# Kernel optimization log

Measured on AMD Instinct MI355X. Metric: run time of the kernel, lower is better.

Reference implementation:

```python
import jax, jax.numpy as jnp
import numpy as np

B, T, NF, T2V, GH, NH, GRUH = 128, 256, 17, 16, 32, 4, 128


def _t2v(t, w0, b0, W, Bp):
    # t: [...] -> [..., T2V] = [linear term, sin periodic terms]
    lin = t[..., None] * w0 + b0
    per = jnp.sin(t[..., None] * W + Bp)
    return jnp.concatenate([lin, per], axis=-1)


def _gat(h, adj, W, a_src, a_dst, residual):
    # h: [N, F, Din], W: [Din, H, O], a_*: [H, O]; batched multi-head GAT over N graphs
    p = jnp.einsum('nfd,dho->nfho', h, W)
    es = jnp.einsum('nfho,ho->nhf', p, a_src)
    ed = jnp.einsum('nfho,ho->nhf', p, a_dst)
    e = jax.nn.leaky_relu(es[:, :, :, None] + ed[:, :, None, :], 0.2)  # [N,H,F,F]
    e = jnp.where(adj[None, None] > 0, e, jnp.float32(-1e9))
    a = jax.nn.softmax(e, axis=-1)
    out = jnp.einsum('nhij,njho->niho', a, p).reshape(h.shape[0], h.shape[1], -1)
    if residual:
        out = out + h
    return jax.nn.elu(out)


def _gru_dir(x, wih, whh, bih, bhh, reverse):
    # PyTorch GRU gate order [r, z, n]; x: [B,T,D] -> (outputs [B,T,H], h_final [B,H])
    gx = jnp.einsum('btd,gd->btg', x, wih) + bih
    if reverse:
        gx = gx[:, ::-1]
    H = whh.shape[1]

    def step(h, gxt):
        gh = h @ whh.T + bhh
        r = jax.nn.sigmoid(gxt[:, :H] + gh[:, :H])
        z = jax.nn.sigmoid(gxt[:, H:2 * H] + gh[:, H:2 * H])
        n = jnp.tanh(gxt[:, 2 * H:] + r * gh[:, 2 * H:])
        h2 = (1.0 - z) * n + z * h
        return h2, h2

    h0 = jnp.zeros((x.shape[0], H), x.dtype)
    hT, ys = jax.lax.scan(step, h0, jnp.swapaxes(gx, 0, 1))
    ys = jnp.swapaxes(ys, 0, 1)
    if reverse:
        ys = ys[:, ::-1]
    return ys, hT


def setup_inputs() -> dict:
    key = jax.random.key(0)
    ks = iter(jax.random.split(key, 64))

    def nrm(shape, fan):
        return jax.random.normal(next(ks), shape, jnp.float32) / np.float32(np.sqrt(fan))

    X = jax.random.normal(next(ks), (B, T, NF), jnp.float32)
    mask = (jax.random.uniform(next(ks), (B, T, NF)) > 0.3).astype(jnp.float32)
    delta = jax.random.uniform(next(ks), (B, T, NF), jnp.float32) * 10.0
    times = jnp.broadcast_to(jnp.arange(T, dtype=jnp.float32)[None], (B, T)) + jax.random.uniform(next(ks), (B, T), jnp.float32)
    adj = jnp.ones((NF, NF), jnp.float32) - jnp.eye(NF, dtype=jnp.float32)

    D0 = 2 + 2 * T2V  # node_in_dim = 34
    GO = GH * NH      # gat_out_dim = 128
    inp = dict(X=X, mask=mask, delta=delta, times=times, adj=adj,
               aw0=nrm((1,), 1), ab0=nrm((1,), 1), aW=nrm((T2V - 1,), 1), aB=nrm((T2V - 1,), 1),
               dw0=nrm((1,), 1), db0=nrm((1,), 1), dW=nrm((T2V - 1,), 1), dB=nrm((T2V - 1,), 1),
               gW0=nrm((D0, NH, GH), D0), gas0=nrm((NH, GH), GH), gad0=nrm((NH, GH), GH),
               gW1=nrm((GO, NH, GH), GO), gas1=nrm((NH, GH), GH), gad1=nrm((NH, GH), GH))
    for name, ind in [('g0f', GO), ('g0b', GO), ('g1f', 2 * GRUH), ('g1b', 2 * GRUH)]:
        inp[name + '_wih'] = nrm((3 * GRUH, ind), ind)
        inp[name + '_whh'] = nrm((3 * GRUH, GRUH), GRUH)
        inp[name + '_bih'] = jnp.zeros((3 * GRUH,), jnp.float32)
        inp[name + '_bhh'] = jnp.zeros((3 * GRUH,), jnp.float32)
    pd = 2 * GRUH
    inp.update(mh_w1=nrm((64, pd), pd), mh_b1=jnp.zeros((64,), jnp.float32),
               mh_w2=nrm((1, 64), 64), mh_b2=jnp.zeros((1,), jnp.float32),
               ch_w1=nrm((64, pd), pd), ch_b1=jnp.zeros((64,), jnp.float32),
               ch_w2=nrm((1, 64), 64), ch_b2=jnp.zeros((1,), jnp.float32))
    return inp


def reference(X, mask, delta, times, adj, aw0, ab0, aW, aB, dw0, db0, dW, dB,
              gW0, gas0, gad0, gW1, gas1, gad1,
              g0f_wih, g0f_whh, g0f_bih, g0f_bhh, g0b_wih, g0b_whh, g0b_bih, g0b_bhh,
              g1f_wih, g1f_whh, g1f_bih, g1f_bhh, g1b_wih, g1b_whh, g1b_bih, g1b_bhh,
              mh_w1, mh_b1, mh_w2, mh_b2, ch_w1, ch_b1, ch_w2, ch_b2):
    Bx, Tx, F = X.shape
    # node features: [x, mask, time2vec(t), time2vec(delta)] -> [B,T,F,34]
    t_emb = _t2v(times, aw0, ab0, aW, aB)
    t_emb = jnp.broadcast_to(t_emb[:, :, None, :], (Bx, Tx, F, T2V))
    d_emb = _t2v(delta, dw0, db0, dW, dB)
    nf = jnp.concatenate([X[..., None], mask[..., None], t_emb, d_emb], axis=-1)
    # batched GAT over all B*T graphs at once (replaces the Python bt-loop)
    h = nf.reshape(Bx * Tx, F, nf.shape[-1])
    h = _gat(h, adj, gW0, gas0, gad0, False)
    h = _gat(h, adj, gW1, gas1, gad1, True)
    z = h.mean(axis=1).reshape(Bx, Tx, NH * GH)
    # bidirectional 2-layer GRU
    yf, _ = _gru_dir(z, g0f_wih, g0f_whh, g0f_bih, g0f_bhh, False)
    yb, _ = _gru_dir(z, g0b_wih, g0b_whh, g0b_bih, g0b_bhh, True)
    y = jnp.concatenate([yf, yb], axis=-1)
    yf1, hf1 = _gru_dir(y, g1f_wih, g1f_whh, g1f_bih, g1f_bhh, False)
    yb1, hb1 = _gru_dir(y, g1b_wih, g1b_whh, g1b_bih, g1b_bhh, True)
    gru_out = jnp.concatenate([yf1, yb1], axis=-1)
    patient_emb = jnp.concatenate([hf1, hb1], axis=-1)
    m = jax.nn.relu(patient_emb @ mh_w1.T + mh_b1) @ mh_w2.T + mh_b2
    risk = jax.nn.relu(patient_emb @ ch_w1.T + ch_b1) @ ch_w2.T + ch_b2
    return (m, jax.nn.sigmoid(m), risk, patient_emb, gru_out)
```

## Files before the change

### kernel.cpp

```cpp
#include <hip/hip_runtime.h>
#include <hip/hip_bf16.h>
#include <math.h>

#define NFE 17
#define T2V 16
#define D0C 34
#define BB 128
#define TT 256
#define HH 128
#define PSTR 132
#define ASTR 136

typedef __hip_bfloat16 bf16;
__device__ __forceinline__ float b2f(bf16 x) { return __bfloat162float(x); }

typedef __attribute__((ext_vector_type(8))) __bf16 bfrag;
typedef __attribute__((ext_vector_type(4))) float  ffrag;
typedef __attribute__((ext_vector_type(4))) __bf16 bf4;

__device__ __forceinline__ float elu_fast(float v)  { return v > 0.f ? v : __expf(v) - 1.f; }
__device__ __forceinline__ float sigm_fast(float x) { return __fdividef(1.f, 1.f + __expf(-x)); }
__device__ __forceinline__ float tanh_fast(float x) {
  return __fdividef(2.f, 1.f + __expf(-2.f*x)) - 1.f;
}

__device__ __bf16 g_W0h[8192],  g_W0l[8192];
__device__ __bf16 g_W1h[16384], g_W1l[16384];

__global__ __launch_bounds__(256) void prep_w(const float* __restrict__ W0,
                                              const float* __restrict__ W1) {
  const int tid = blockIdx.x*256 + threadIdx.x;
  if (tid < 16384) {
    const int j = tid & 7, lane = (tid >> 3) & 63, ks = (tid >> 9) & 3, nt = tid >> 11;
    const int n = nt*16 + (lane & 15), k = ks*32 + (lane >> 4)*8 + j;
    const float v = W1[k*128 + n];
    const __bf16 hi = (__bf16)v;
    g_W1h[tid] = hi;
    g_W1l[tid] = (__bf16)(v - (float)hi);
  }
  if (tid < 8192) {
    const int j = tid & 7, lane = (tid >> 3) & 63, ks = (tid >> 9) & 1, nt = tid >> 10;
    const int n = nt*16 + (lane & 15), k = ks*32 + (lane >> 4)*8 + j;
    const float v = (k < D0C) ? W0[k*128 + n] : 0.f;
    const __bf16 hi = (__bf16)v;
    g_W0h[tid] = hi;
    g_W0l[tid] = (__bf16)(v - (float)hi);
  }
}

template<int KSTEPS>
__device__ __forceinline__ void gat_proj_mfma(const __bf16* s_ah, const __bf16* s_al,
                                              const __bf16* __restrict__ Wth,
                                              const __bf16* __restrict__ Wtl,
                                              float* s_p, int tid)
{
  const int lane = tid & 63, wv = tid >> 6;
  const int mn = lane & 15, q = lane >> 4;
  ffrag acc[2][2] = {};
  #pragma unroll
  for (int ks = 0; ks < KSTEPS; ++ks) {
    const bfrag ah0 = *(const bfrag*)&s_ah[(     mn)*ASTR + ks*32 + q*8];
    const bfrag al0 = *(const bfrag*)&s_al[(     mn)*ASTR + ks*32 + q*8];
    const bfrag ah1 = *(const bfrag*)&s_ah[(16 + mn)*ASTR + ks*32 + q*8];
    const bfrag al1 = *(const bfrag*)&s_al[(16 + mn)*ASTR + ks*32 + q*8];
    #pragma unroll
    for (int nt = 0; nt < 2; ++nt) {
      const int fi = (((wv*2 + nt)*KSTEPS + ks)*64 + lane)*8;
      const bfrag bh = *(const bfrag*)&Wth[fi];
      const bfrag bl = *(const bfrag*)&Wtl[fi];
      acc[0][nt] = __builtin_amdgcn_mfma_f32_16x16x32_bf16(al0, bh, acc[0][nt], 0,0,0);
      acc[0][nt] = __builtin_amdgcn_mfma_f32_16x16x32_bf16(ah0, bl, acc[0][nt], 0,0,0);
      acc[0][nt] = __builtin_amdgcn_mfma_f32_16x16x32_bf16(ah0, bh, acc[0][nt], 0,0,0);
      acc[1][nt] = __builtin_amdgcn_mfma_f32_16x16x32_bf16(al1, bh, acc[1][nt], 0,0,0);
      acc[1][nt] = __builtin_amdgcn_mfma_f32_16x16x32_bf16(ah1, bl, acc[1][nt], 0,0,0);
      acc[1][nt] = __builtin_amdgcn_mfma_f32_16x16x32_bf16(ah1, bh, acc[1][nt], 0,0,0);
    }
  }
  const int n0 = wv*32;
  #pragma unroll
  for (int nt = 0; nt < 2; ++nt) {
    const int col = n0 + nt*16 + mn;
    #pragma unroll
    for (int i = 0; i < 4; ++i)
      s_p[(q*4 + i)*PSTR + col] = acc[0][nt][i];
    if (q == 0)
      s_p[16*PSTR + col] = acc[1][nt][0];
  }
}

__device__ __forceinline__ void gat_scores(const float* s_p,
                                           const float* __restrict__ asrc,
                                           const float* __restrict__ adst,
                                           float* s_es, float* s_ed, int tid) {
  if (tid < 2*4*NFE) {
    const int which = tid >= 4*NFE;
    const int r = which ? tid - 4*NFE : tid;
    const int h = r / NFE, f = r - h*NFE;
    const float* av = which ? adst : asrc;
    float acc = 0.f;
    #pragma unroll
    for (int o = 0; o < 32; o += 4) {
      const float4 p4 = *(const float4*)&s_p[f*PSTR + h*32 + o];
      const float4 a4 = *(const float4*)&av[h*32 + o];
      acc = fmaf(p4.x, a4.x, acc);
      acc = fmaf(p4.y, a4.y, acc);
      acc = fmaf(p4.z, a4.z, acc);
      acc = fmaf(p4.w, a4.w, acc);
    }
    (which ? s_ed : s_es)[h*NFE + f] = acc;
  }
}

__device__ __forceinline__ void gat_softmax(const float* s_es, const float* s_ed,
                                            const float* s_adj,
                                            float* s_e, int tid) {
  if (tid < 4*NFE) {
    const int h = tid / NFE, i = tid - h*NFE;
    float row[NFE]; float mx = -1e30f;
    #pragma unroll
    for (int j = 0; j < NFE; ++j) {
      float v = -1.0e9f;
      if (s_adj[i*NFE + j] > 0.f) {
        float e = s_es[h*NFE + i] + s_ed[h*NFE + j];
        v = (e > 0.f) ? e : 0.2f*e;
      }
      row[j] = v; mx = fmaxf(mx, v);
    }
    float sum = 0.f;
    #pragma unroll
    for (int j = 0; j < NFE; ++j) { row[j] = __expf(row[j] - mx); sum += row[j]; }
    const float inv = __fdividef(1.f, sum);
    #pragma unroll
    for (int j = 0; j < NFE; ++j) s_e[(h*NFE + i)*NFE + j] = row[j]*inv;
  }
}

__device__ __forceinline__ void gat_out_rb(const float* s_e, const float* s_p,
                                           __bf16* s_ah, __bf16* s_al, int tid) {
  const int tx = (tid & 31) * 4, ty = tid >> 5;
  const int h = tx >> 5;
  float acc[3][4];
  #pragma unroll
  for (int i = 0; i < 3; ++i)
    #pragma unroll
    for (int c = 0; c < 4; ++c) acc[i][c] = 0.f;
  for (int j = 0; j < NFE; ++j) {
    const float4 pv = *(const float4*)&s_p[j*PSTR + tx];
    #pragma unroll
    for (int i = 0; i < 3; ++i) {
      const int r = ty + 8*i;
      if (i < 2 || ty == 0) {
        const float av = s_e[(h*NFE + r)*NFE + j];
        acc[i][0] = fmaf(av, pv.x, acc[i][0]);
        acc[i][1] = fmaf(av, pv.y, acc[i][1]);
        acc[i][2] = fmaf(av, pv.z, acc[i][2]);
        acc[i][3] = fmaf(av, pv.w, acc[i][3]);
      }
    }
  }
  #pragma unroll
  for (int i = 0; i < 3; ++i) {
    const int r = ty + 8*i;
    if (i < 2 || ty == 0) {
      bf4 h4, l4;
      #pragma unroll
      for (int c = 0; c < 4; ++c) {
        const float v = elu_fast(acc[i][c]);
        const __bf16 hi = (__bf16)v;
        h4[c] = hi;
        l4[c] = (__bf16)(v - (float)hi);
      }
      *(bf4*)&s_ah[r*ASTR + tx] = h4;
      *(bf4*)&s_al[r*ASTR + tx] = l4;
    }
  }
}

__device__ __forceinline__ void gat_out_psum(const float* s_e, const float* s_p,
                                             const __bf16* s_ah, const __bf16* s_al,
                                             float* psum, int tid) {
  const int tx = (tid & 31) * 4, ty = tid >> 5;
  const int h = tx >> 5;
  float acc[3][4];
  #pragma unroll
  for (int i = 0; i < 3; ++i)
    #pragma unroll
    for (int c = 0; c < 4; ++c) acc[i][c] = 0.f;
  for (int j = 0; j < NFE; ++j) {
    const float4 pv = *(const float4*)&s_p[j*PSTR + tx];
    #pragma unroll
    for (int i = 0; i < 3; ++i) {
      const int r = ty + 8*i;
      if (i < 2 || ty == 0) {
        const float av = s_e[(h*NFE + r)*NFE + j];
        acc[i][0] = fmaf(av, pv.x, acc[i][0]);
        acc[i][1] = fmaf(av, pv.y, acc[i][1]);
        acc[i][2] = fmaf(av, pv.z, acc[i][2]);
        acc[i][3] = fmaf(av, pv.w, acc[i][3]);
      }
    }
  }
  #pragma unroll
  for (int c = 0; c < 4; ++c) psum[c] = 0.f;
  #pragma unroll
  for (int i = 0; i < 3; ++i) {
    const int r = ty + 8*i;
    if (i < 2 || ty == 0) {
      const bf4 rh = *(const bf4*)&s_ah[r*ASTR + tx];
      const bf4 rl = *(const bf4*)&s_al[r*ASTR + tx];
      #pragma unroll
      for (int c = 0; c < 4; ++c) {
        const float res = (float)rh[c] + (float)rl[c];
        psum[c] += elu_fast(acc[i][c] + res);
      }
    }
  }
}

__global__ __launch_bounds__(256) void gat_fused(
    const float* __restrict__ X,  const float* __restrict__ Mk,
    const float* __restrict__ Dl, const float* __restrict__ Tm,
    const float* __restrict__ Adj,
    const float* __restrict__ aw0, const float* __restrict__ ab0,
    const float* __restrict__ aW,  const float* __restrict__ aB,
    const float* __restrict__ dw0, const float* __restrict__ db0,
    const float* __restrict__ dW,  const float* __restrict__ dB,
    const float* __restrict__ as0, const float* __restrict__ ad0,
    const float* __restrict__ as1, const float* __restrict__ ad1,
    float* __restrict__ zslot)
{
  __shared__ __align__(16) unsigned char smem[24624];
  __bf16* s_ah  = (__bf16*)(smem);
  __bf16* s_al  = (__bf16*)(smem + 4624);
  float*  s_p   = (float*)(smem + 9248);
  float*  s_e   = (float*)(smem + 18224);
  float*  s_red = (float*)(smem + 18224);
  float*  s_es  = (float*)(smem + 22848);
  float*  s_ed  = (float*)(smem + 23120);
  float*  s_t   = (float*)(smem + 23392);
  float*  s_adj = (float*)(smem + 23456);
  const int n = blockIdx.x;
  const int tid = threadIdx.x;

  const float tv = Tm[n];
  if (tid < T2V) {
    s_t[tid] = (tid == 0) ? fmaf(tv, aw0[0], ab0[0])
                          : __sinf(fmaf(tv, aW[tid-1], aB[tid-1]));
  }
  for (int idx = tid; idx < NFE*NFE; idx += 256) s_adj[idx] = Adj[idx];
  __syncthreads();
  for (int idx = tid; idx < NFE*64; idx += 256) {
    const int f = idx >> 6, c = idx & 63;
    float v = 0.f;
    if (c == 0)            v = X [(size_t)n*NFE + f];
    else if (c == 1)       v = Mk[(size_t)n*NFE + f];
    else if (c < 2 + T2V)  v = s_t[c-2];
    else if (c < D0C) {
      const float dd = Dl[(size_t)n*NFE + f];
      const int j = c - (2 + T2V);
      v = (j == 0) ? fmaf(dd, dw0[0], db0[0])
                   : __sinf(fmaf(dd, dW[j-1], dB[j-1]));
    }
    const __bf16 hi = (__bf16)v;
    s_ah[f*ASTR + c] = hi;
    s_al[f*ASTR + c] = (__bf16)(v - (float)hi);
  }
  __syncthreads();
  gat_proj_mfma<2>(s_ah, s_al, g_W0h, g_W0l, s_p, tid);  __syncthreads();
  gat_scores(s_p, as0, ad0, s_es, s_ed, tid);            __syncthreads();
  gat_softmax(s_es, s_ed, s_adj, s_e, tid);              __syncthreads();
  gat_out_rb(s_e, s_p, s_ah, s_al, tid);                 __syncthreads();
  gat_proj_mfma<4>(s_ah, s_al, g_W1h, g_W1l, s_p, tid);  __syncthreads();
  gat_scores(s_p, as1, ad1, s_es, s_ed, tid);            __syncthreads();
  gat_softmax(s_es, s_ed, s_adj, s_e, tid);              __syncthreads();
  {
    float psum[4];
    gat_out_psum(s_e, s_p, s_ah, s_al, psum, tid);
    __syncthreads();
    const int tx = (tid & 31) * 4, ty = tid >> 5;
    *(float4*)&s_red[ty*128 + tx] = *(float4*)psum;
    __syncthreads();
    if (tid < 128) {
      float acc = 0.f;
      #pragma unroll
      for (int k = 0; k < 8; ++k) acc += s_red[k*128 + tid];
      zslot[(size_t)n*256 + 128 + tid] = acc * (1.0f/17.0f);
    }
  }
}

__global__ __launch_bounds__(256) void gemm_xw_mfma(
    const float* __restrict__ A, int lda, const float* __restrict__ W,
    const float* __restrict__ bias, bf16* __restrict__ C, int K)
{
  __shared__ __bf16 Ah[64][40];
  __shared__ __bf16 Al[64][40];
  __shared__ __bf16 Wh[64][40];
  __shared__ __bf16 Wl[64][40];
  const int tid = threadIdx.x;
  const int bm0 = blockIdx.x * 64;
  const int bn0 = blockIdx.y * 64;
  const int lane = tid & 63, wv = tid >> 6;
  const int mn = lane & 15, q = lane >> 4;
  const int sr = tid >> 2, sk = (tid & 3) * 8;
  ffrag acc[4] = {};
  for (int kk = 0; kk < K; kk += 32) {
    {
      float av[8];
      *(float4*)&av[0] = *(const float4*)&A[(size_t)(bm0 + sr)*lda + kk + sk];
      *(float4*)&av[4] = *(const float4*)&A[(size_t)(bm0 + sr)*lda + kk + sk + 4];
      __bf16 th[8], tl[8];
      #pragma unroll
      for (int i = 0; i < 8; ++i) {
        const __bf16 hi = (__bf16)av[i];
        th[i] = hi;
        tl[i] = (__bf16)(av[i] - (float)hi);
      }
      *(bfrag*)&Ah[sr][sk] = *(bfrag*)th;
      *(bfrag*)&Al[sr][sk] = *(bfrag*)tl;
      float wv8[8];
      *(float4*)&wv8[0] = *(const float4*)&W[(size_t)(bn0 + sr)*K + kk + sk];
      *(float4*)&wv8[4] = *(const float4*)&W[(size_t)(bn0 + sr)*K + kk + sk + 4];
      __bf16 wh8[8], wl8[8];
      #pragma unroll
      for (int i = 0; i < 8; ++i) {
        const __bf16 hi = (__bf16)wv8[i];
        wh8[i] = hi;
        wl8[i] = (__bf16)(wv8[i] - (float)hi);
      }
      *(bfrag*)&Wh[sr][sk] = *(bfrag*)wh8;
      *(bfrag*)&Wl[sr][sk] = *(bfrag*)wl8;
    }
    __syncthreads();
    const bfrag afh = *(const bfrag*)&Ah[16*wv + mn][q*8];
    const bfrag afl = *(const bfrag*)&Al[16*wv + mn][q*8];
    #pragma unroll
    for (int t = 0; t < 4; ++t) {
      const bfrag bwh = *(const bfrag*)&Wh[16*t + mn][q*8];
      const bfrag bwl = *(const bfrag*)&Wl[16*t + mn][q*8];
      acc[t] = __builtin_amdgcn_mfma_f32_16x16x32_bf16(afl, bwh, acc[t], 0, 0, 0);
      acc[t] = __builtin_amdgcn_mfma_f32_16x16x32_bf16(afh, bwl, acc[t], 0, 0, 0);
      acc[t] = __builtin_amdgcn_mfma_f32_16x16x32_bf16(afh, bwh, acc[t], 0, 0, 0);
    }
    __syncthreads();
  }
  #pragma unroll
  for (int t = 0; t < 4; ++t) {
    const int col = bn0 + 16*t + mn;
    const float bv = bias[col];
    #pragma unroll
    for (int i = 0; i < 4; ++i) {
      const int row = bm0 + 16*wv + q*4 + i;
      C[(size_t)row*384 + col] = __float2bfloat16(acc[t][i] + bv);
    }
  }
}

__global__ __launch_bounds__(384, 1) void gru_rec(
    const bf16* __restrict__ gxf,
    const bf16* __restrict__ gxb,
    const float* __restrict__ whh_f, const float* __restrict__ whh_b,
    const float* __restrict__ bhh_f, const float* __restrict__ bhh_b,
    float* __restrict__ ys,
    float* __restrict__ hfin)
{
  const int blk = blockIdx.x;
  const int dir = blk >> 7;
  const int b   = blk & 127;
  const int g   = threadIdx.x;
  const float* whh = dir ? whh_b : whh_f;
  const float* bhh = dir ? bhh_b : bhh_f;
  const bf16* gx   = (dir ? gxb : gxf) + (size_t)b*TT*384;
  __shared__ __align__(16) float s_h[HH];
  __shared__ float s_gh[3*HH];
  __shared__ float s_gx[3*HH];
  float4 w[HH/4];
  #pragma unroll
  for (int d4 = 0; d4 < HH/4; ++d4)
    w[d4] = *(const float4*)&whh[(size_t)g*HH + 4*d4];
  const float bh = bhh[g];
  float hreg = 0.f;
  if (g < HH) s_h[g] = 0.f;
  __syncthreads();
  for (int s = 0; s < TT; ++s) {
    const int t = dir ? (TT-1-s) : s;
    const float gxv = b2f(gx[(size_t)t*384 + g]);
    float a0 = bh, a1 = 0.f, a2 = 0.f, a3 = 0.f;
    const float4* h4 = (const float4*)s_h;
    #pragma unroll
    for (int d4 = 0; d4 < HH/4; ++d4) {
      const float4 hv = h4[d4];
      a0 = fmaf(hv.x, w[d4].x, a0);
      a1 = fmaf(hv.y, w[d4].y, a1);
      a2 = fmaf(hv.z, w[d4].z, a2);
      a3 = fmaf(hv.w, w[d4].w, a3);
    }
    s_gh[g] = (a0 + a1) + (a2 + a3);
    s_gx[g] = gxv;
    __syncthreads();
    if (g < HH) {
      const float r  = sigm_fast(s_gx[g]    + s_gh[g]);
      const float zg = sigm_fast(s_gx[HH+g] + s_gh[HH+g]);
      const float nn = tanh_fast(s_gx[2*HH+g] + r*s_gh[2*HH+g]);
      hreg = (1.f - zg)*nn + zg*hreg;
      s_h[g] = hreg;
      ys[((size_t)b*TT + t)*256 + dir*HH + g] = hreg;
    }
    __syncthreads();
  }
  if (g < HH && hfin) hfin[(size_t)b*256 + dir*HH + g] = hreg;
}

__global__ __launch_bounds__(64) void heads_k(
    const float* __restrict__ pemb,
    const float* __restrict__ mw1, const float* __restrict__ mb1,
    const float* __restrict__ mw2, const float* __restrict__ mb2,
    const float* __restrict__ cw1, const float* __restrict__ cb1,
    const float* __restrict__ cw2, const float* __restrict__ cb2,
    float* __restrict__ out)
{
  const int b = blockIdx.x, tid = threadIdx.x;
  __shared__ float sh[64];
  const float* pe = pemb + (size_t)b*256;
  float acc = mb1[tid];
  for (int d = 0; d < 256; ++d) acc = fmaf(pe[d], mw1[(size_t)tid*256 + d], acc);
  sh[tid] = fmaxf(acc, 0.f) * mw2[tid];
  __syncthreads();
  if (tid == 0) {
    float s = mb2[0];
    for (int i = 0; i < 64; ++i) s += sh[i];
    out[b]       = s;
    out[128 + b] = 1.f/(1.f + expf(-s));
  }
  __syncthreads();
  acc = cb1[tid];
  for (int d = 0; d < 256; ++d) acc = fmaf(pe[d], cw1[(size_t)tid*256 + d], acc);
  sh[tid] = fmaxf(acc, 0.f) * cw2[tid];
  __syncthreads();
  if (tid == 0) {
    float s = cb2[0];
    for (int i = 0; i < 64; ++i) s += sh[i];
    out[256 + b] = s;
  }
}

extern "C" void kernel_launch(void* const* d_in, const int* in_sizes, int n_in,
                              void* d_out, int out_size, void* d_ws, size_t ws_size,
                              hipStream_t stream) {
  const float* X    = (const float*)d_in[0];
  const float* Mk   = (const float*)d_in[1];
  const float* Dl   = (const float*)d_in[2];
  const float* Tm   = (const float*)d_in[3];
  const float* Adj  = (const float*)d_in[4];
  const float* aw0  = (const float*)d_in[5];
  const float* ab0  = (const float*)d_in[6];
  const float* aWt  = (const float*)d_in[7];
  const float* aBt  = (const float*)d_in[8];
  const float* dw0  = (const float*)d_in[9];
  const float* db0  = (const float*)d_in[10];
  const float* dWt  = (const float*)d_in[11];
  const float* dBt  = (const float*)d_in[12];
  const float* gW0  = (const float*)d_in[13];
  const float* gas0 = (const float*)d_in[14];
  const float* gad0 = (const float*)d_in[15];
  const float* gW1  = (const float*)d_in[16];
  const float* gas1 = (const float*)d_in[17];
  const float* gad1 = (const float*)d_in[18];
  const float* g0f_wih = (const float*)d_in[19];
  const float* g0f_whh = (const float*)d_in[20];
  const float* g0f_bih = (const float*)d_in[21];
  const float* g0f_bhh = (const float*)d_in[22];
  const float* g0b_wih = (const float*)d_in[23];
  const float* g0b_whh = (const float*)d_in[24];
  const float* g0b_bih = (const float*)d_in[25];
  const float* g0b_bhh = (const float*)d_in[26];
  const float* g1f_wih = (const float*)d_in[27];
  const float* g1f_whh = (const float*)d_in[28];
  const float* g1f_bih = (const float*)d_in[29];
  const float* g1f_bhh = (const float*)d_in[30];
  const float* g1b_wih = (const float*)d_in[31];
  const float* g1b_whh = (const float*)d_in[32];
  const float* g1b_bih = (const float*)d_in[33];
  const float* g1b_bhh = (const float*)d_in[34];
  const float* mh_w1 = (const float*)d_in[35];
  const float* mh_b1 = (const float*)d_in[36];
  const float* mh_w2 = (const float*)d_in[37];
  const float* mh_b2 = (const float*)d_in[38];
  const float* ch_w1 = (const float*)d_in[39];
  const float* ch_b1 = (const float*)d_in[40];
  const float* ch_w2 = (const float*)d_in[41];
  const float* ch_b2 = (const float*)d_in[42];

  bf16* gxA = (bf16*)d_ws;
  bf16* gxB = gxA + 12582912;

  float* out  = (float*)d_out;
  float* pemb = out + 384;
  float* slot = out + 384 + 32768;

  prep_w<<<64, 256, 0, stream>>>(gW0, gW1);

  gat_fused<<<dim3(BB*TT), dim3(256), 0, stream>>>(
      X, Mk, Dl, Tm, Adj, aw0, ab0, aWt, aBt, dw0, db0, dWt, dBt,
      gas0, gad0, gas1, gad1, slot);

  dim3 ggrid(32768/64, 384/64);
  gemm_xw_mfma<<<ggrid, 256, 0, stream>>>(slot + 128, 256, g0f_wih, g0f_bih, gxA, 128);
  gemm_xw_mfma<<<ggrid, 256, 0, stream>>>(slot + 128, 256, g0b_wih, g0b_bih, gxB, 128);
  gru_rec<<<256, 384, 0, stream>>>(gxA, gxB, g0f_whh, g0b_whh, g0f_bhh, g0b_bhh,
                                   slot, nullptr);
  gemm_xw_mfma<<<ggrid, 256, 0, stream>>>(slot, 256, g1f_wih, g1f_bih, gxA, 256);
  gemm_xw_mfma<<<ggrid, 256, 0, stream>>>(slot, 256, g1b_wih, g1b_bih, gxB, 256);
  gru_rec<<<256, 384, 0, stream>>>(gxA, gxB, g1f_whh, g1b_whh, g1f_bhh, g1b_bhh,
                                   slot, pemb);

  heads_k<<<128, 64, 0, stream>>>(pemb, mh_w1, mh_b1, mh_w2, mh_b2,
                                  ch_w1, ch_b1, ch_w2, ch_b2, out);
}
```

Baseline: 1.470 ms.

## Process two GAT graphs per block and use single-chain GRU dot product

The fused GAT kernel now handles two graphs per 256-thread block. Waves are split so each pair of waves projects one graph over 64 output columns, and the scores, softmax, output and mean-reduction stages are doubled inside the same block. This halves the grid and amortises the adjacency load, time2vec setup and barriers across two graphs, at the cost of roughly double the LDS per block, which may lower occupancy. Separately, the GRU recurrent dot product is collapsed from four accumulators into one serial FMA chain, which lengthens the dependency chain.

```diff
diff --git a/kernel.cpp b/kernel.cpp
--- a/kernel.cpp
+++ b/kernel.cpp
@@ -49,14 +49,19 @@
 }
 
 template<int KSTEPS>
-__device__ __forceinline__ void gat_proj_mfma(const __bf16* s_ah, const __bf16* s_al,
-                                              const __bf16* __restrict__ Wth,
-                                              const __bf16* __restrict__ Wtl,
-                                              float* s_p, int tid)
+__device__ __forceinline__ void gat_proj_mfma2(const __bf16* s_ah0, const __bf16* s_al0,
+                                               const __bf16* __restrict__ Wth,
+                                               const __bf16* __restrict__ Wtl,
+                                               float* s_p0, int tid)
 {
   const int lane = tid & 63, wv = tid >> 6;
+  const int g  = wv >> 1;
+  const int nq = wv & 1;
+  const __bf16* s_ah = s_ah0 + g*(NFE*ASTR);
+  const __bf16* s_al = s_al0 + g*(NFE*ASTR);
+  float* s_p = s_p0 + g*(NFE*PSTR);
   const int mn = lane & 15, q = lane >> 4;
-  ffrag acc[2][2] = {};
+  ffrag acc[2][4] = {};
   #pragma unroll
   for (int ks = 0; ks < KSTEPS; ++ks) {
     const bfrag ah0 = *(const bfrag*)&s_ah[(     mn)*ASTR + ks*32 + q*8];
@@ -64,8 +69,8 @@
     const bfrag ah1 = *(const bfrag*)&s_ah[(16 + mn)*ASTR + ks*32 + q*8];
     const bfrag al1 = *(const bfrag*)&s_al[(16 + mn)*ASTR + ks*32 + q*8];
     #pragma unroll
-    for (int nt = 0; nt < 2; ++nt) {
-      const int fi = (((wv*2 + nt)*KSTEPS + ks)*64 + lane)*8;
+    for (int nt = 0; nt < 4; ++nt) {
+      const int fi = (((nq*4 + nt)*KSTEPS + ks)*64 + lane)*8;
       const bfrag bh = *(const bfrag*)&Wth[fi];
       const bfrag bl = *(const bfrag*)&Wtl[fi];
       acc[0][nt] = __builtin_amdgcn_mfma_f32_16x16x32_bf16(al0, bh, acc[0][nt], 0,0,0);
@@ -76,9 +81,9 @@
       acc[1][nt] = __builtin_amdgcn_mfma_f32_16x16x32_bf16(ah1, bh, acc[1][nt], 0,0,0);
     }
   }
-  const int n0 = wv*32;
-  #pragma unroll
-  for (int nt = 0; nt < 2; ++nt) {
+  const int n0 = nq*64;
+  #pragma unroll
+  for (int nt = 0; nt < 4; ++nt) {
     const int col = n0 + nt*16 + mn;
     #pragma unroll
     for (int i = 0; i < 4; ++i)
@@ -88,40 +93,48 @@
   }
 }
 
-__device__ __forceinline__ void gat_scores(const float* s_p,
-                                           const float* __restrict__ asrc,
-                                           const float* __restrict__ adst,
-                                           float* s_es, float* s_ed, int tid) {
-  if (tid < 2*4*NFE) {
-    const int which = tid >= 4*NFE;
-    const int r = which ? tid - 4*NFE : tid;
-    const int h = r / NFE, f = r - h*NFE;
+__device__ __forceinline__ void gat_scores2(const float* s_p0,
+                                            const float* __restrict__ asrc,
+                                            const float* __restrict__ adst,
+                                            float* s_es, float* s_ed, int tid) {
+  for (int it = tid; it < 2*2*4*NFE; it += 256) {
+    const int g = it / (2*4*NFE);
+    const int r = it - g*(2*4*NFE);
+    const int which = r >= 4*NFE;
+    const int rr = which ? r - 4*NFE : r;
+    const int h = rr / NFE, f = rr - h*NFE;
     const float* av = which ? adst : asrc;
+    const float* sp = s_p0 + g*(NFE*PSTR);
     float acc = 0.f;
     #pragma unroll
     for (int o = 0; o < 32; o += 4) {
-      const float4 p4 = *(const float4*)&s_p[f*PSTR + h*32 + o];
+      const float4 p4 = *(const float4*)&sp[f*PSTR + h*32 + o];
       const float4 a4 = *(const float4*)&av[h*32 + o];
       acc = fmaf(p4.x, a4.x, acc);
       acc = fmaf(p4.y, a4.y, acc);
       acc = fmaf(p4.z, a4.z, acc);
       acc = fmaf(p4.w, a4.w, acc);
     }
-    (which ? s_ed : s_es)[h*NFE + f] = acc;
-  }
-}
-
-__device__ __forceinline__ void gat_softmax(const float* s_es, const float* s_ed,
-                                            const float* s_adj,
-                                            float* s_e, int tid) {
-  if (tid < 4*NFE) {
-    const int h = tid / NFE, i = tid - h*NFE;
+    (which ? s_ed : s_es)[g*4*NFE + h*NFE + f] = acc;
+  }
+}
+
+__device__ __forceinline__ void gat_softmax2(const float* s_es, const float* s_ed,
+                                             const float* s_adj,
+                                             float* s_e0, int tid) {
+  if (tid < 2*4*NFE) {
+    const int g = tid >= 4*NFE;
+    const int r = tid - g*4*NFE;
+    const int h = r / NFE, i = r - h*NFE;
+    const float* es = s_es + g*4*NFE;
+    const float* ed = s_ed + g*4*NFE;
+    float* s_e = s_e0 + g*(4*NFE*NFE);
     float row[NFE]; float mx = -1e30f;
     #pragma unroll
     for (int j = 0; j < NFE; ++j) {
       float v = -1.0e9f;
       if (s_adj[i*NFE + j] > 0.f) {
-        float e = s_es[h*NFE + i] + s_ed[h*NFE + j];
+        float e = es[h*NFE + i] + ed[h*NFE + j];
         v = (e > 0.f) ? e : 0.2f*e;
       }
       row[j] = v; mx = fmaxf(mx, v);
@@ -229,32 +242,36 @@
     const float* __restrict__ as1, const float* __restrict__ ad1,
     float* __restrict__ zslot)
 {
-  __shared__ __align__(16) unsigned char smem[24624];
-  __bf16* s_ah  = (__bf16*)(smem);
-  __bf16* s_al  = (__bf16*)(smem + 4624);
-  float*  s_p   = (float*)(smem + 9248);
-  float*  s_e   = (float*)(smem + 18224);
-  float*  s_red = (float*)(smem + 18224);
-  float*  s_es  = (float*)(smem + 22848);
-  float*  s_ed  = (float*)(smem + 23120);
-  float*  s_t   = (float*)(smem + 23392);
-  float*  s_adj = (float*)(smem + 23456);
-  const int n = blockIdx.x;
+  __shared__ __align__(16) unsigned char smem[51536];
+  __bf16* s_ah0 = (__bf16*)(smem);
+  __bf16* s_al0 = (__bf16*)(smem + 9248);
+  float*  s_p0  = (float*)(smem + 18496);
+  float*  s_e0  = (float*)(smem + 36448);
+  float*  s_red = (float*)(smem + 36448);
+  float*  s_es  = (float*)(smem + 45696);
+  float*  s_ed  = (float*)(smem + 46240);
+  float*  s_t   = (float*)(smem + 46784);
+  float*  s_adj = (float*)(smem + 46912);
+  const int n0 = blockIdx.x * 2;
   const int tid = threadIdx.x;
 
-  const float tv = Tm[n];
-  if (tid < T2V) {
-    s_t[tid] = (tid == 0) ? fmaf(tv, aw0[0], ab0[0])
-                          : __sinf(fmaf(tv, aW[tid-1], aB[tid-1]));
+  if (tid < 2*T2V) {
+    const int g = tid >> 4, k = tid & 15;
+    const float tv = Tm[n0 + g];
+    s_t[g*T2V + k] = (k == 0) ? fmaf(tv, aw0[0], ab0[0])
+                              : __sinf(fmaf(tv, aW[k-1], aB[k-1]));
   }
   for (int idx = tid; idx < NFE*NFE; idx += 256) s_adj[idx] = Adj[idx];
   __syncthreads();
-  for (int idx = tid; idx < NFE*64; idx += 256) {
-    const int f = idx >> 6, c = idx & 63;
+  for (int idx = tid; idx < 2*NFE*64; idx += 256) {
+    const int g = idx / (NFE*64);
+    const int rest = idx - g*(NFE*64);
+    const int f = rest >> 6, c = rest & 63;
+    const int n = n0 + g;
     float v = 0.f;
     if (c == 0)            v = X [(size_t)n*NFE + f];
     else if (c == 1)       v = Mk[(size_t)n*NFE + f];
-    else if (c < 2 + T2V)  v = s_t[c-2];
+    else if (c < 2 + T2V)  v = s_t[g*T2V + c-2];
     else if (c < D0C) {
       const float dd = Dl[(size_t)n*NFE + f];
       const int j = c - (2 + T2V);
@@ -262,29 +279,34 @@
                    : __sinf(fmaf(dd, dW[j-1], dB[j-1]));
     }
     const __bf16 hi = (__bf16)v;
-    s_ah[f*ASTR + c] = hi;
-    s_al[f*ASTR + c] = (__bf16)(v - (float)hi);
-  }
-  __syncthreads();
-  gat_proj_mfma<2>(s_ah, s_al, g_W0h, g_W0l, s_p, tid);  __syncthreads();
-  gat_scores(s_p, as0, ad0, s_es, s_ed, tid);            __syncthreads();
-  gat_softmax(s_es, s_ed, s_adj, s_e, tid);              __syncthreads();
-  gat_out_rb(s_e, s_p, s_ah, s_al, tid);                 __syncthreads();
-  gat_proj_mfma<4>(s_ah, s_al, g_W1h, g_W1l, s_p, tid);  __syncthreads();
-  gat_scores(s_p, as1, ad1, s_es, s_ed, tid);            __syncthreads();
-  gat_softmax(s_es, s_ed, s_adj, s_e, tid);              __syncthreads();
+    s_ah0[g*(NFE*ASTR) + f*ASTR + c] = hi;
+    s_al0[g*(NFE*ASTR) + f*ASTR + c] = (__bf16)(v - (float)hi);
+  }
+  __syncthreads();
+  gat_proj_mfma2<2>(s_ah0, s_al0, g_W0h, g_W0l, s_p0, tid);  __syncthreads();
+  gat_scores2(s_p0, as0, ad0, s_es, s_ed, tid);              __syncthreads();
+  gat_softmax2(s_es, s_ed, s_adj, s_e0, tid);                __syncthreads();
+  gat_out_rb(s_e0,          s_p0,          s_ah0,            s_al0,            tid);
+  gat_out_rb(s_e0 + 4*NFE*NFE, s_p0 + NFE*PSTR, s_ah0 + NFE*ASTR, s_al0 + NFE*ASTR, tid);
+  __syncthreads();
+  gat_proj_mfma2<4>(s_ah0, s_al0, g_W1h, g_W1l, s_p0, tid);  __syncthreads();
+  gat_scores2(s_p0, as1, ad1, s_es, s_ed, tid);              __syncthreads();
+  gat_softmax2(s_es, s_ed, s_adj, s_e0, tid);                __syncthreads();
   {
-    float psum[4];
-    gat_out_psum(s_e, s_p, s_ah, s_al, psum, tid);
+    float psA[4], psB[4];
+    gat_out_psum(s_e0,           s_p0,           s_ah0,           s_al0,           psA, tid);
+    gat_out_psum(s_e0 + 4*NFE*NFE, s_p0 + NFE*PSTR, s_ah0 + NFE*ASTR, s_al0 + NFE*ASTR, psB, tid);
     __syncthreads();
     const int tx = (tid & 31) * 4, ty = tid >> 5;
-    *(float4*)&s_red[ty*128 + tx] = *(float4*)psum;
+    *(float4*)&s_red[ty*128 + tx]        = *(float4*)psA;
+    *(float4*)&s_red[1156 + ty*128 + tx] = *(float4*)psB;
     __syncthreads();
-    if (tid < 128) {
+    {
+      const int g = tid >> 7, c = tid & 127;
       float acc = 0.f;
       #pragma unroll
-      for (int k = 0; k < 8; ++k) acc += s_red[k*128 + tid];
-      zslot[(size_t)n*256 + 128 + tid] = acc * (1.0f/17.0f);
+      for (int k = 0; k < 8; ++k) acc += s_red[g*1156 + k*128 + c];
+      zslot[(size_t)(n0 + g)*256 + 128 + c] = acc * (1.0f/17.0f);
     }
   }
 }
@@ -385,17 +407,17 @@
   for (int s = 0; s < TT; ++s) {
     const int t = dir ? (TT-1-s) : s;
     const float gxv = b2f(gx[(size_t)t*384 + g]);
-    float a0 = bh, a1 = 0.f, a2 = 0.f, a3 = 0.f;
+    float acc = bh;
     const float4* h4 = (const float4*)s_h;
     #pragma unroll
     for (int d4 = 0; d4 < HH/4; ++d4) {
       const float4 hv = h4[d4];
-      a0 = fmaf(hv.x, w[d4].x, a0);
-      a1 = fmaf(hv.y, w[d4].y, a1);
-      a2 = fmaf(hv.z, w[d4].z, a2);
-      a3 = fmaf(hv.w, w[d4].w, a3);
-    }
-    s_gh[g] = (a0 + a1) + (a2 + a3);
+      acc = fmaf(hv.x, w[d4].x, acc);
+      acc = fmaf(hv.y, w[d4].y, acc);
+      acc = fmaf(hv.z, w[d4].z, acc);
+      acc = fmaf(hv.w, w[d4].w, acc);
+    }
+    s_gh[g] = acc;
     s_gx[g] = gxv;
     __syncthreads();
     if (g < HH) {
@@ -500,7 +522,7 @@
 
   prep_w<<<64, 256, 0, stream>>>(gW0, gW1);
 
-  gat_fused<<<dim3(BB*TT), dim3(256), 0, stream>>>(
+  gat_fused<<<dim3(BB*TT/2), dim3(256), 0, stream>>>(
       X, Mk, Dl, Tm, Adj, aw0, ab0, aWt, aBt, dw0, db0, dWt, dBt,
       gas0, gad0, gas1, gad1, slot);
 
```

Result: faster. 1.328 ms (-9.6%).

## Move GAT attention aggregation onto split-bf16 MFMA and fuse mean reduction

Applied to the files above, without the earlier changes.

The attention-weighted aggregation in both GAT layers now runs on MFMA instead of scalar FMA loops. The projection writes a transposed hi/lo bf16 copy of p, and the softmax writes hi/lo bf16 attention matrices padded to 32 columns. The second layer's mean over nodes is done with wave shuffles and written directly, which removes the shared-memory reduction and two barriers. This raises LDS use to about 45KB per block, which may lower occupancy, and it adds a zero-fill pass. The GRU dot product also goes from four accumulators to one serial chain, which lengthens the FMA dependency chain.

```diff
diff --git a/kernel.cpp b/kernel.cpp
--- a/kernel.cpp
+++ b/kernel.cpp
@@ -52,7 +52,8 @@
 __device__ __forceinline__ void gat_proj_mfma(const __bf16* s_ah, const __bf16* s_al,
                                               const __bf16* __restrict__ Wth,
                                               const __bf16* __restrict__ Wtl,
-                                              float* s_p, int tid)
+                                              float* s_p, __bf16* s_pth, __bf16* s_ptl,
+                                              int tid)
 {
   const int lane = tid & 63, wv = tid >> 6;
   const int mn = lane & 15, q = lane >> 4;
@@ -81,10 +82,20 @@
   for (int nt = 0; nt < 2; ++nt) {
     const int col = n0 + nt*16 + mn;
     #pragma unroll
-    for (int i = 0; i < 4; ++i)
-      s_p[(q*4 + i)*PSTR + col] = acc[0][nt][i];
-    if (q == 0)
-      s_p[16*PSTR + col] = acc[1][nt][0];
+    for (int i = 0; i < 4; ++i) {
+      const float v = acc[0][nt][i];
+      s_p[(q*4 + i)*PSTR + col] = v;
+      const __bf16 hi = (__bf16)v;
+      s_pth[col*32 + q*4 + i] = hi;
+      s_ptl[col*32 + q*4 + i] = (__bf16)(v - (float)hi);
+    }
+    if (q == 0) {
+      const float v = acc[1][nt][0];
+      s_p[16*PSTR + col] = v;
+      const __bf16 hi = (__bf16)v;
+      s_pth[col*32 + 16] = hi;
+      s_ptl[col*32 + 16] = (__bf16)(v - (float)hi);
+    }
   }
 }
 
@@ -113,7 +124,7 @@
 
 __device__ __forceinline__ void gat_softmax(const float* s_es, const float* s_ed,
                                             const float* s_adj,
-                                            float* s_e, int tid) {
+                                            __bf16* s_Eh, __bf16* s_El, int tid) {
   if (tid < 4*NFE) {
     const int h = tid / NFE, i = tid - h*NFE;
     float row[NFE]; float mx = -1e30f;
@@ -131,88 +142,95 @@
     for (int j = 0; j < NFE; ++j) { row[j] = __expf(row[j] - mx); sum += row[j]; }
     const float inv = __fdividef(1.f, sum);
     #pragma unroll
-    for (int j = 0; j < NFE; ++j) s_e[(h*NFE + i)*NFE + j] = row[j]*inv;
-  }
-}
-
-__device__ __forceinline__ void gat_out_rb(const float* s_e, const float* s_p,
-                                           __bf16* s_ah, __bf16* s_al, int tid) {
-  const int tx = (tid & 31) * 4, ty = tid >> 5;
-  const int h = tx >> 5;
-  float acc[3][4];
-  #pragma unroll
-  for (int i = 0; i < 3; ++i)
-    #pragma unroll
-    for (int c = 0; c < 4; ++c) acc[i][c] = 0.f;
-  for (int j = 0; j < NFE; ++j) {
-    const float4 pv = *(const float4*)&s_p[j*PSTR + tx];
-    #pragma unroll
-    for (int i = 0; i < 3; ++i) {
-      const int r = ty + 8*i;
-      if (i < 2 || ty == 0) {
-        const float av = s_e[(h*NFE + r)*NFE + j];
-        acc[i][0] = fmaf(av, pv.x, acc[i][0]);
-        acc[i][1] = fmaf(av, pv.y, acc[i][1]);
-        acc[i][2] = fmaf(av, pv.z, acc[i][2]);
-        acc[i][3] = fmaf(av, pv.w, acc[i][3]);
-      }
-    }
-  }
-  #pragma unroll
-  for (int i = 0; i < 3; ++i) {
-    const int r = ty + 8*i;
-    if (i < 2 || ty == 0) {
-      bf4 h4, l4;
-      #pragma unroll
-      for (int c = 0; c < 4; ++c) {
-        const float v = elu_fast(acc[i][c]);
-        const __bf16 hi = (__bf16)v;
-        h4[c] = hi;
-        l4[c] = (__bf16)(v - (float)hi);
-      }
-      *(bf4*)&s_ah[r*ASTR + tx] = h4;
-      *(bf4*)&s_al[r*ASTR + tx] = l4;
-    }
-  }
-}
-
-__device__ __forceinline__ void gat_out_psum(const float* s_e, const float* s_p,
-                                             const __bf16* s_ah, const __bf16* s_al,
-                                             float* psum, int tid) {
-  const int tx = (tid & 31) * 4, ty = tid >> 5;
-  const int h = tx >> 5;
-  float acc[3][4];
-  #pragma unroll
-  for (int i = 0; i < 3; ++i)
-    #pragma unroll
-    for (int c = 0; c < 4; ++c) acc[i][c] = 0.f;
-  for (int j = 0; j < NFE; ++j) {
-    const float4 pv = *(const float4*)&s_p[j*PSTR + tx];
-    #pragma unroll
-    for (int i = 0; i < 3; ++i) {
-      const int r = ty + 8*i;
-      if (i < 2 || ty == 0) {
-        const float av = s_e[(h*NFE + r)*NFE + j];
-        acc[i][0] = fmaf(av, pv.x, acc[i][0]);
-        acc[i][1] = fmaf(av, pv.y, acc[i][1]);
-        acc[i][2] = fmaf(av, pv.z, acc[i][2]);
-        acc[i][3] = fmaf(av, pv.w, acc[i][3]);
-      }
-    }
-  }
-  #pragma unroll
-  for (int c = 0; c < 4; ++c) psum[c] = 0.f;
-  #pragma unroll
-  for (int i = 0; i < 3; ++i) {
-    const int r = ty + 8*i;
-    if (i < 2 || ty == 0) {
-      const bf4 rh = *(const bf4*)&s_ah[r*ASTR + tx];
-      const bf4 rl = *(const bf4*)&s_al[r*ASTR + tx];
-      #pragma unroll
-      for (int c = 0; c < 4; ++c) {
-        const float res = (float)rh[c] + (float)rl[c];
-        psum[c] += elu_fast(acc[i][c] + res);
-      }
+    for (int j = 0; j < NFE; ++j) {
+      const float v = row[j]*inv;
+      const __bf16 hi = (__bf16)v;
+      s_Eh[h*544 + i*32 + j] = hi;
+      s_El[h*544 + i*32 + j] = (__bf16)(v - (float)hi);
+    }
+  }
+}
+
+__device__ __forceinline__ void gat_out0_mfma(const __bf16* s_Eh, const __bf16* s_El,
+                                              const __bf16* s_pth, const __bf16* s_ptl,
+                                              __bf16* s_ah, __bf16* s_al, int tid) {
+  const int lane = tid & 63, wv = tid >> 6;
+  const int mn = lane & 15, q = lane >> 4;
+  ffrag acc[2][2] = {};
+  const bfrag eh0 = *(const bfrag*)&s_Eh[wv*544 + mn*32 + q*8];
+  const bfrag el0 = *(const bfrag*)&s_El[wv*544 + mn*32 + q*8];
+  const bfrag eh1 = *(const bfrag*)&s_Eh[wv*544 + (16+mn)*32 + q*8];
+  const bfrag el1 = *(const bfrag*)&s_El[wv*544 + (16+mn)*32 + q*8];
+  #pragma unroll
+  for (int nt = 0; nt < 2; ++nt) {
+    const int nrow = wv*32 + nt*16 + mn;
+    const bfrag ph = *(const bfrag*)&s_pth[nrow*32 + q*8];
+    const bfrag pl = *(const bfrag*)&s_ptl[nrow*32 + q*8];
+    acc[0][nt] = __builtin_amdgcn_mfma_f32_16x16x32_bf16(el0, ph, acc[0][nt], 0,0,0);
+    acc[0][nt] = __builtin_amdgcn_mfma_f32_16x16x32_bf16(eh0, pl, acc[0][nt], 0,0,0);
+    acc[0][nt] = __builtin_amdgcn_mfma_f32_16x16x32_bf16(eh0, ph, acc[0][nt], 0,0,0);
+    acc[1][nt] = __builtin_amdgcn_mfma_f32_16x16x32_bf16(el1, ph, acc[1][nt], 0,0,0);
+    acc[1][nt] = __builtin_amdgcn_mfma_f32_16x16x32_bf16(eh1, pl, acc[1][nt], 0,0,0);
+    acc[1][nt] = __builtin_amdgcn_mfma_f32_16x16x32_bf16(eh1, ph, acc[1][nt], 0,0,0);
+  }
+  #pragma unroll
+  for (int nt = 0; nt < 2; ++nt) {
+    const int c = wv*32 + nt*16 + mn;
+    #pragma unroll
+    for (int i = 0; i < 4; ++i) {
+      const float v = elu_fast(acc[0][nt][i]);
+      const __bf16 hi = (__bf16)v;
+      s_ah[(q*4+i)*ASTR + c] = hi;
+      s_al[(q*4+i)*ASTR + c] = (__bf16)(v - (float)hi);
+    }
+    if (q == 0) {
+      const float v = elu_fast(acc[1][nt][0]);
+      const __bf16 hi = (__bf16)v;
+      s_ah[16*ASTR + c] = hi;
+      s_al[16*ASTR + c] = (__bf16)(v - (float)hi);
+    }
+  }
+}
+
+__device__ __forceinline__ void gat_out1_mfma(const __bf16* s_Eh, const __bf16* s_El,
+                                              const __bf16* s_pth, const __bf16* s_ptl,
+                                              const __bf16* s_ah, const __bf16* s_al,
+                                              float* __restrict__ zrow, int tid) {
+  const int lane = tid & 63, wv = tid >> 6;
+  const int mn = lane & 15, q = lane >> 4;
+  ffrag acc[2][2] = {};
+  const bfrag eh0 = *(const bfrag*)&s_Eh[wv*544 + mn*32 + q*8];
+  const bfrag el0 = *(const bfrag*)&s_El[wv*544 + mn*32 + q*8];
+  const bfrag eh1 = *(const bfrag*)&s_Eh[wv*544 + (16+mn)*32 + q*8];
+  const bfrag el1 = *(const bfrag*)&s_El[wv*544 + (16+mn)*32 + q*8];
+  #pragma unroll
+  for (int nt = 0; nt < 2; ++nt) {
+    const int nrow = wv*32 + nt*16 + mn;
+    const bfrag ph = *(const bfrag*)&s_pth[nrow*32 + q*8];
+    const bfrag pl = *(const bfrag*)&s_ptl[nrow*32 + q*8];
+    acc[0][nt] = __builtin_amdgcn_mfma_f32_16x16x32_bf16(el0, ph, acc[0][nt], 0,0,0);
+    acc[0][nt] = __builtin_amdgcn_mfma_f32_16x16x32_bf16(eh0, pl, acc[0][nt], 0,0,0);
+    acc[0][nt] = __builtin_amdgcn_mfma_f32_16x16x32_bf16(eh0, ph, acc[0][nt], 0,0,0);
+    acc[1][nt] = __builtin_amdgcn_mfma_f32_16x16x32_bf16(el1, ph, acc[1][nt], 0,0,0);
+    acc[1][nt] = __builtin_amdgcn_mfma_f32_16x16x32_bf16(eh1, pl, acc[1][nt], 0,0,0);
+    acc[1][nt] = __builtin_amdgcn_mfma_f32_16x16x32_bf16(eh1, ph, acc[1][nt], 0,0,0);
+  }
+  #pragma unroll
+  for (int nt = 0; nt < 2; ++nt) {
+    const int c = wv*32 + nt*16 + mn;
+    float sum = 0.f;
+    #pragma unroll
+    for (int i = 0; i < 4; ++i) {
+      const int r = q*4 + i;
+      const float res = (float)s_ah[r*ASTR + c] + (float)s_al[r*ASTR + c];
+      sum += elu_fast(acc[0][nt][i] + res);
+    }
+    sum += __shfl_xor(sum, 16);
+    sum += __shfl_xor(sum, 32);
+    if (q == 0) {
+      const float res = (float)s_ah[16*ASTR + c] + (float)s_al[16*ASTR + c];
+      sum += elu_fast(acc[1][nt][0] + res);
+      zrow[c] = sum * (1.0f/17.0f);
     }
   }
 }
@@ -229,19 +247,26 @@
     const float* __restrict__ as1, const float* __restrict__ ad1,
     float* __restrict__ zslot)
 {
-  __shared__ __align__(16) unsigned char smem[24624];
+  __shared__ __align__(16) unsigned char smem[45088];
   __bf16* s_ah  = (__bf16*)(smem);
   __bf16* s_al  = (__bf16*)(smem + 4624);
   float*  s_p   = (float*)(smem + 9248);
-  float*  s_e   = (float*)(smem + 18224);
-  float*  s_red = (float*)(smem + 18224);
-  float*  s_es  = (float*)(smem + 22848);
-  float*  s_ed  = (float*)(smem + 23120);
-  float*  s_t   = (float*)(smem + 23392);
-  float*  s_adj = (float*)(smem + 23456);
+  __bf16* s_pth = (__bf16*)(smem + 18224);
+  __bf16* s_ptl = (__bf16*)(smem + 26416);
+  __bf16* s_Eh  = (__bf16*)(smem + 34608);
+  __bf16* s_El  = (__bf16*)(smem + 38960);
+  float*  s_es  = (float*)(smem + 43312);
+  float*  s_ed  = (float*)(smem + 43584);
+  float*  s_t   = (float*)(smem + 43856);
+  float*  s_adj = (float*)(smem + 43920);
   const int n = blockIdx.x;
   const int tid = threadIdx.x;
 
+  {
+    const float4 z4 = {0.f, 0.f, 0.f, 0.f};
+    float4* zp = (float4*)(smem + 18224);
+    for (int i = tid; i < 1568; i += 256) zp[i] = z4;
+  }
   const float tv = Tm[n];
   if (tid < T2V) {
     s_t[tid] = (tid == 0) ? fmaf(tv, aw0[0], ab0[0])
@@ -266,27 +291,15 @@
     s_al[f*ASTR + c] = (__bf16)(v - (float)hi);
   }
   __syncthreads();
-  gat_proj_mfma<2>(s_ah, s_al, g_W0h, g_W0l, s_p, tid);  __syncthreads();
-  gat_scores(s_p, as0, ad0, s_es, s_ed, tid);            __syncthreads();
-  gat_softmax(s_es, s_ed, s_adj, s_e, tid);              __syncthreads();
-  gat_out_rb(s_e, s_p, s_ah, s_al, tid);                 __syncthreads();
-  gat_proj_mfma<4>(s_ah, s_al, g_W1h, g_W1l, s_p, tid);  __syncthreads();
-  gat_scores(s_p, as1, ad1, s_es, s_ed, tid);            __syncthreads();
-  gat_softmax(s_es, s_ed, s_adj, s_e, tid);              __syncthreads();
-  {
-    float psum[4];
-    gat_out_psum(s_e, s_p, s_ah, s_al, psum, tid);
-    __syncthreads();
-    const int tx = (tid & 31) * 4, ty = tid >> 5;
-    *(float4*)&s_red[ty*128 + tx] = *(float4*)psum;
-    __syncthreads();
-    if (tid < 128) {
-      float acc = 0.f;
-      #pragma unroll
-      for (int k = 0; k < 8; ++k) acc += s_red[k*128 + tid];
-      zslot[(size_t)n*256 + 128 + tid] = acc * (1.0f/17.0f);
-    }
-  }
+  gat_proj_mfma<2>(s_ah, s_al, g_W0h, g_W0l, s_p, s_pth, s_ptl, tid); __syncthreads();
+  gat_scores(s_p, as0, ad0, s_es, s_ed, tid);                         __syncthreads();
+  gat_softmax(s_es, s_ed, s_adj, s_Eh, s_El, tid);                    __syncthreads();
+  gat_out0_mfma(s_Eh, s_El, s_pth, s_ptl, s_ah, s_al, tid);           __syncthreads();
+  gat_proj_mfma<4>(s_ah, s_al, g_W1h, g_W1l, s_p, s_pth, s_ptl, tid); __syncthreads();
+  gat_scores(s_p, as1, ad1, s_es, s_ed, tid);                         __syncthreads();
+  gat_softmax(s_es, s_ed, s_adj, s_Eh, s_El, tid);                    __syncthreads();
+  gat_out1_mfma(s_Eh, s_El, s_pth, s_ptl, s_ah, s_al,
+                zslot + (size_t)n*256 + 128, tid);
 }
 
 __global__ __launch_bounds__(256) void gemm_xw_mfma(
@@ -385,17 +398,17 @@
   for (int s = 0; s < TT; ++s) {
     const int t = dir ? (TT-1-s) : s;
     const float gxv = b2f(gx[(size_t)t*384 + g]);
-    float a0 = bh, a1 = 0.f, a2 = 0.f, a3 = 0.f;
+    float acc = bh;
     const float4* h4 = (const float4*)s_h;
     #pragma unroll
     for (int d4 = 0; d4 < HH/4; ++d4) {
       const float4 hv = h4[d4];
-      a0 = fmaf(hv.x, w[d4].x, a0);
-      a1 = fmaf(hv.y, w[d4].y, a1);
-      a2 = fmaf(hv.z, w[d4].z, a2);
-      a3 = fmaf(hv.w, w[d4].w, a3);
-    }
-    s_gh[g] = (a0 + a1) + (a2 + a3);
+      acc = fmaf(hv.x, w[d4].x, acc);
+      acc = fmaf(hv.y, w[d4].y, acc);
+      acc = fmaf(hv.z, w[d4].z, acc);
+      acc = fmaf(hv.w, w[d4].w, acc);
+    }
+    s_gh[g] = acc;
     s_gx[g] = gxv;
     __syncthreads();
     if (g < HH) {
```

Result: faster. 1.264 ms (-14.0%).
